# Kernel tuning notes

Measured on AMD Instinct MI355X. Metric: run time of the kernel, lower is better.

Reference implementation:

```python
import jax, jax.numpy as jnp
import numpy as np

H, L, N = 512, 4096, 64

def make_dplr_hippo(n):
    # HiPPO-LegS -> NPLR -> DPLR diagonalization (numpy, init-time only)
    p0 = np.sqrt(1 + 2 * np.arange(n))
    A = p0[:, None] * p0[None, :]
    A = -(np.tril(A) - np.diag(np.arange(n)))
    p = np.sqrt(np.arange(n) + 0.5)
    b = np.sqrt(2 * np.arange(n) + 1.0)
    S = A + p[:, None] * p[None, :]
    Lambda_re = np.full(n, np.diagonal(S).mean())
    Lambda_im, V = np.linalg.eigh(S * -1j)
    Pc = V.conj().T @ p
    Bc = V.conj().T @ b
    return Lambda_re, Lambda_im, Pc, Bc

def setup_inputs() -> dict:
    key = jax.random.key(0)
    k_u, k_c, k_s = jax.random.split(key, 3)
    lr, li, Pc, Bc = make_dplr_hippo(N)
    tile = lambda v: jnp.tile(jnp.asarray(v, jnp.float32)[None, :], (H, 1))
    dt_min, dt_max = 0.001, 0.1
    log_step = (jax.random.uniform(k_s, (H, 1), jnp.float32)
                * (np.log(dt_max) - np.log(dt_min)) + np.log(dt_min))
    return {
        "u": jax.random.normal(k_u, (H, L), jnp.float32),
        "Lambda_re": tile(lr), "Lambda_im": tile(li),
        "P_re": tile(Pc.real), "P_im": tile(Pc.imag),
        "B_re": tile(Bc.real), "B_im": tile(Bc.imag),
        "C": jax.random.normal(k_c, (H, N, 2), jnp.float32) * (0.5 ** 0.5),
        "D": jnp.ones((H, 1), jnp.float32),
        "log_step": log_step,
    }

def reference(u, Lambda_re, Lambda_im, P_re, P_im, B_re, B_im, C, D, log_step):
    # u: [H, L]; all params leading dim H (vmapped channels)
    Lam = jnp.minimum(Lambda_re, -1e-4) + 1j * Lambda_im      # [H, N]
    P = P_re + 1j * P_im                                       # [H, N]
    B = B_re + 1j * B_im                                       # [H, N]
    Cc = C[..., 0] + 1j * C[..., 1]                             # [H, N]
    step = jnp.exp(log_step)                                    # [H, 1]
    Lseq = u.shape[-1]
    Omega = jnp.exp(-2j * jnp.pi * (jnp.arange(Lseq) / Lseq)).astype(jnp.complex64)  # [L]
    g = (2.0 / step) * ((1.0 - Omega) / (1.0 + Omega))[None, :]  # [H, L]
    c = 2.0 / (1.0 + Omega)                                      # [L]
    denom = 1.0 / (g[:, :, None] - Lam[:, None, :])              # [H, L, N]
    cauchy = lambda v: jnp.einsum('hn,hln->hl', v, denom)
    k00 = cauchy(Cc.conj() * B)
    k01 = cauchy(Cc.conj() * P)
    k10 = cauchy(P.conj() * B)
    k11 = cauchy(P.conj() * P)
    atRoots = c[None, :] * (k00 - k01 * (1.0 / (1.0 + k11)) * k10)
    K = jnp.fft.ifft(atRoots, Lseq, axis=-1).real                # [H, L] conv kernel
    # causal convolution via zero-padded FFT (length 2L)
    ud = jnp.fft.rfft(u, n=2 * Lseq, axis=-1)
    Kd = jnp.fft.rfft(K, n=2 * Lseq, axis=-1)
    y = jnp.fft.irfft(ud * Kd, n=2 * Lseq, axis=-1)[..., :Lseq]
    return y + D * u
```

## Files before the change

kernel.cpp:

```cpp
#include <hip/hip_runtime.h>
#include <math.h>

#define NT 512

typedef float v2 __attribute__((ext_vector_type(2)));

__device__ __forceinline__ v2 vrot(v2 a){ return (v2){-a.y, a.x}; }
__device__ __forceinline__ v2 vconj(v2 a){ return (v2){a.x, -a.y}; }
__device__ __forceinline__ v2 vcmul(v2 a, v2 b){ return a.x*b + a.y*vrot(b); }
__device__ __forceinline__ v2 vfma1(float s, v2 v, v2 acc){
    return (v2){ __builtin_fmaf(s, v.x, acc.x), __builtin_fmaf(s, v.y, acc.y) };
}

__device__ __forceinline__ int SW(int e){ return e ^ (((e>>5) ^ (e>>9)) & 15); }

__device__ __forceinline__ int d8r4(int x){
    return ((x&7)<<9) | (((x>>3)&7)<<6) | (((x>>6)&7)<<3) | ((x>>9)&7);
}

__device__ __forceinline__ void dft8_inv(v2 t[8], v2 y[8]) {
    const float RH = 0.70710678f;
    v2 p  = t[0]+t[4], m  = t[0]-t[4], q  = t[2]+t[6], r  = t[2]-t[6];
    v2 rr = vrot(r);
    v2 E0 = p+q, E2 = p-q, E1 = m+rr, E3 = m-rr;
    v2 p2 = t[1]+t[5], m2 = t[1]-t[5], q2 = t[3]+t[7], r2 = t[3]-t[7];
    v2 rr2 = vrot(r2);
    v2 O0 = p2+q2, O2 = p2-q2, O1 = m2+rr2, O3 = m2-rr2;
    v2 W1O = RH*(O1 + vrot(O1));
    v2 W2O = vrot(O2);
    v2 W3O = vrot(RH*(O3 + vrot(O3)));
    y[0] = E0 + O0;  y[4] = E0 - O0;
    y[1] = E1 + W1O; y[5] = E1 - W1O;
    y[2] = E2 + W2O; y[6] = E2 - W2O;
    y[3] = E3 + W3O; y[7] = E3 - W3O;
}

__device__ __forceinline__ void dft8_fwd(v2 t[8], v2 y[8]) {
    const float RH = 0.70710678f;
    v2 p  = t[0]+t[4], m  = t[0]-t[4], q  = t[2]+t[6], r  = t[2]-t[6];
    v2 rr = vrot(r);
    v2 E0 = p+q, E2 = p-q, E1 = m-rr, E3 = m+rr;
    v2 p2 = t[1]+t[5], m2 = t[1]-t[5], q2 = t[3]+t[7], r2 = t[3]-t[7];
    v2 rr2 = vrot(r2);
    v2 O0 = p2+q2, O2 = p2-q2, O1 = m2-rr2, O3 = m2+rr2;
    v2 W1O = RH*(O1 - vrot(O1));
    v2 W2O = (v2){O2.y, -O2.x};
    v2 W3O = (-RH)*(O3 + vrot(O3));
    y[0] = E0 + O0;  y[4] = E0 - O0;
    y[1] = E1 + W1O; y[5] = E1 - W1O;
    y[2] = E2 + W2O; y[6] = E2 - W2O;
    y[3] = E3 + W3O; y[7] = E3 - W3O;
}

template<int Q, bool TW>
__device__ __forceinline__ void r8_dit_inv(v2* buf, int tid) {
    int j = tid & (Q-1);
    int base = 8*tid - 7*j;
    v2 t[8];
    #pragma unroll
    for (int k = 0; k < 8; ++k) t[k] = buf[SW(base + k*Q)];
    if (TW) {
        const float fm = 6.2831853072f / (float)(8*Q);
        float sb, cb; __sincosf(fm*(float)j, &sb, &cb);
        v2 W1 = (v2){cb, sb};
        v2 W2 = vcmul(W1,W1), W3 = vcmul(W1,W2), W4 = vcmul(W2,W2),
           W5 = vcmul(W2,W3), W6 = vcmul(W3,W3), W7 = vcmul(W3,W4);
        t[1]=vcmul(t[1],W1); t[2]=vcmul(t[2],W2); t[3]=vcmul(t[3],W3);
        t[4]=vcmul(t[4],W4); t[5]=vcmul(t[5],W5); t[6]=vcmul(t[6],W6);
        t[7]=vcmul(t[7],W7);
    }
    v2 y[8];
    dft8_inv(t, y);
    #pragma unroll
    for (int m = 0; m < 8; ++m) buf[SW(base + m*Q)] = y[m];
    __syncthreads();
}

template<int Q>
__device__ __forceinline__ void r8_dif_fwd(v2* buf, int tid) {
    int j = tid & (Q-1);
    int baseL = 8*tid - 7*j;
    v2 W1=(v2){1.0f,0.0f},W2=W1,W3=W1,W4=W1,W5=W1,W6=W1,W7=W1;
    if (Q > 1) {
        const float fm = -6.2831853072f / (float)(8*Q);
        float sb, cb; __sincosf(fm*(float)j, &sb, &cb);
        W1 = (v2){cb, sb};
        W2 = vcmul(W1,W1); W3 = vcmul(W1,W2); W4 = vcmul(W2,W2);
        W5 = vcmul(W2,W3); W6 = vcmul(W3,W3); W7 = vcmul(W3,W4);
    }
    #pragma unroll 1
    for (int hh = 0; hh < 2; ++hh) {
        int base = baseL + (hh << 12);
        v2 t[8];
        #pragma unroll
        for (int k = 0; k < 8; ++k) t[k] = buf[SW(base + k*Q)];
        v2 y[8];
        dft8_fwd(t, y);
        if (Q > 1) {
            y[1]=vcmul(y[1],W1); y[2]=vcmul(y[2],W2); y[3]=vcmul(y[3],W3);
            y[4]=vcmul(y[4],W4); y[5]=vcmul(y[5],W5); y[6]=vcmul(y[6],W6);
            y[7]=vcmul(y[7],W7);
        }
        #pragma unroll
        for (int m = 0; m < 8; ++m) buf[SW(base + m*Q)] = y[m];
    }
    __syncthreads();
}

__global__ void __launch_bounds__(NT)
s4_fused(const float* __restrict__ u,
         const float* __restrict__ Lre, const float* __restrict__ Lim,
         const float* __restrict__ Pre, const float* __restrict__ Pim,
         const float* __restrict__ Bre, const float* __restrict__ Bim,
         const float* __restrict__ Cin, const float* __restrict__ Din,
         const float* __restrict__ logstep,
         float* __restrict__ out)
{
    __shared__ v2 buf[8192];
    const int tid = threadIdx.x;
    const int h = blockIdx.x;

    v2* par = buf + 4096;
    if (tid < 64) {
        const int n = tid;
        float lre = fminf(Lre[h*64+n], -1e-4f);
        float lim = Lim[h*64+n];
        par[n] = (v2){lre, lim};
        float pr = Pre[h*64+n], pi = Pim[h*64+n];
        float br = Bre[h*64+n], bi = Bim[h*64+n];
        float cr = Cin[h*128+2*n], ci = Cin[h*128+2*n+1];
        v2 cc = (v2){cr, -ci};
        par[64+n]  = vcmul(cc, (v2){br, bi});
        par[128+n] = vcmul(cc, (v2){pr, pi});
        v2 pc = (v2){pr, -pi};
        par[192+n] = vcmul(pc, (v2){br, bi});
        par[256+n] = (v2){pr*pr + pi*pi, 0.0f};
    }
    __syncthreads();

    const float step = expf(logstep[h]);
    const float tos  = 2.0f / step;

    #pragma unroll 1
    for (int hp = 0; hp < 2; ++hp) {
        v2 g[4], cf[4], k00[4], k01[4], k10[4], k11[4];
        const int lbase = hp*(4*NT);
        #pragma unroll
        for (int i = 0; i < 4; ++i) {
            int l = lbase + i*NT + tid;
            float ang = -6.2831855f * ((float)l * (1.0f/4096.0f));
            double ds, dc;
            sincos((double)ang, &ds, &dc);
            float Omx = (float)dc, Omy = (float)ds;
            float nx = 1.0f-Omx, ny = -Omy;
            float dx = 1.0f+Omx, dy =  Omy;
            float dinv = 1.0f/(dx*dx + dy*dy);
            g[i]  = (v2){tos*((nx*dx+ny*dy)*dinv), tos*((ny*dx-nx*dy)*dinv)};
            cf[i] = (v2){2.0f*dx*dinv, -2.0f*dy*dinv};
            k00[i]=(v2)(0.0f); k01[i]=(v2)(0.0f); k10[i]=(v2)(0.0f); k11[i]=(v2)(0.0f);
        }
        #pragma unroll 1
        for (int n = 0; n < 64; ++n) {
            v2 lam = par[n];
            v2 w00 = par[64+n], w01 = par[128+n], w10 = par[192+n];
            float w11r = par[256+n].x;
            #pragma unroll
            for (int i = 0; i < 4; ++i) {
                v2 d = g[i] - lam;
                float inv = __builtin_amdgcn_rcpf(d.x*d.x + d.y*d.y);
                v2 p  = d * inv;
                v2 cp = (v2){p.x, -p.y};
                v2 rp = (v2){p.y,  p.x};
                k00[i] = vfma1(w00.y, rp, vfma1(w00.x, cp, k00[i]));
                k01[i] = vfma1(w01.y, rp, vfma1(w01.x, cp, k01[i]));
                k10[i] = vfma1(w10.y, rp, vfma1(w10.x, cp, k10[i]));
                k11[i] = vfma1(w11r,  cp, k11[i]);
            }
        }
        #pragma unroll
        for (int i = 0; i < 4; ++i) {
            int l = lbase + i*NT + tid;
            v2 opk = (v2){1.0f + k11[i].x, k11[i].y};
            float iv = 1.0f/(opk.x*opk.x + opk.y*opk.y);
            v2 r11 = vconj(opk) * iv;
            v2 t  = vcmul(vcmul(k01[i], r11), k10[i]);
            buf[SW(d8r4(l))] = vcmul(cf[i], k00[i] - t);
        }
    }
    __syncthreads();

    r8_dit_inv<1,  false>(buf, tid);
    r8_dit_inv<8,  true >(buf, tid);
    r8_dit_inv<64, true >(buf, tid);
    r8_dit_inv<512,true >(buf, tid);

    {
        float kv[8], uval[8];
        #pragma unroll
        for (int i = 0; i < 8; ++i) {
            int l = i*NT + tid;
            kv[i]   = buf[SW(l)].x * (1.0f/4096.0f);
            uval[i] = u[h*4096 + l];
        }
        __syncthreads();
        #pragma unroll
        for (int i = 0; i < 8; ++i) {
            int l = i*NT + tid;
            buf[SW(l)]      = (v2){uval[i], kv[i]};
            buf[SW(l+4096)] = (v2)(0.0f);
        }
    }
    __syncthreads();

    {
        const float fm = -6.2831853072f / 8192.0f;
        #pragma unroll 1
        for (int i = 0; i < 8; ++i) {
            int j = i*NT + tid;
            float sb, cb; __sincosf(fm*(float)j, &sb, &cb);
            v2 W = (v2){cb, sb};
            int a0 = SW(j), a1 = SW(j+4096);
            v2 a = buf[a0], c = buf[a1];
            buf[a0] = a + c;
            buf[a1] = vcmul(a - c, W);
        }
        __syncthreads();
    }
    r8_dif_fwd<512>(buf, tid);
    r8_dif_fwd<64 >(buf, tid);
    r8_dif_fwd<8  >(buf, tid);
    r8_dif_fwd<1  >(buf, tid);

    {
        const float fm = 6.2831853072f / 8192.0f;
        v2 v[8];
        #pragma unroll 1
        for (int i = 0; i < 8; ++i) {
            int r  = i*NT + tid;
            float sw_, cw_; __sincosf(fm*(float)r, &sw_, &cw_);
            v2 cur = (v2){cw_, sw_};
            int k1 = r,        k1c = (8192 - r) & 8191;
            int k2 = r + 4096, k2c = 4096 - r;
            v2 za = buf[SW(((k1 &1)<<12) + d8r4(k1 >>1))];
            v2 zb = buf[SW(((k1c&1)<<12) + d8r4(k1c>>1))];
            v2 zc = buf[SW(((k2 &1)<<12) + d8r4(k2 >>1))];
            v2 zd = buf[SW(((k2c&1)<<12) + d8r4(k2c>>1))];
            v2 U1 = 0.5f*(za + vconj(zb));
            v2 K1 = -0.5f*vrot(za - vconj(zb));
            v2 Yr = vcmul(U1, K1);
            v2 U2 = 0.5f*(zc + vconj(zd));
            v2 K2 = -0.5f*vrot(zc - vconj(zd));
            v2 Ys = vcmul(U2, K2);
            v[i] = (Yr + Ys) + vrot(vcmul(cur, Yr - Ys));
        }
        __syncthreads();
        #pragma unroll
        for (int i = 0; i < 8; ++i) {
            int r = i*NT + tid;
            buf[SW(d8r4(r))] = v[i];
        }
        __syncthreads();
    }

    r8_dit_inv<1,  false>(buf, tid);
    r8_dit_inv<8,  true >(buf, tid);
    r8_dit_inv<64, true >(buf, tid);
    r8_dit_inv<512,true >(buf, tid);

    {
        const float Dh = Din[h];
        const float sc = 1.0f / 8192.0f;
        const v2* u2 = (const v2*)(u + h*4096);
        v2*     out2 = (v2*)(out + h*4096);
        #pragma unroll
        for (int i = 0; i < 4; ++i) {
            int n = i*NT + tid;
            v2 p  = buf[SW(n)];
            v2 uu = u2[n];
            out2[n] = sc*p + Dh*uu;
        }
    }
}

extern "C" void kernel_launch(void* const* d_in, const int* in_sizes, int n_in,
                              void* d_out, int out_size, void* d_ws, size_t ws_size,
                              hipStream_t stream)
{
    const float* u       = (const float*)d_in[0];
    const float* Lre     = (const float*)d_in[1];
    const float* Lim     = (const float*)d_in[2];
    const float* Pre     = (const float*)d_in[3];
    const float* Pim     = (const float*)d_in[4];
    const float* Bre     = (const float*)d_in[5];
    const float* Bim     = (const float*)d_in[6];
    const float* Cin     = (const float*)d_in[7];
    const float* Din     = (const float*)d_in[8];
    const float* logstep = (const float*)d_in[9];
    float* out = (float*)d_out;
    const int H = in_sizes[8];
    hipLaunchKernelGGL(s4_fused, dim3(H), dim3(NT), 0, stream,
                       u, Lre, Lim, Pre, Pim, Bre, Bim, Cin, Din, logstep, out);
}
```

Measured before the change: 173.3 us.

## Fuse first and last radix-8 FFT stages with adjacent register phases

The first inverse-FFT radix-8 stage now runs directly on register results from the Cauchy phase, so one shared-memory round trip and barrier go away. The last inverse stage is fused with the packing of u and the kernel into the 8192-point input, with the first DIF twiddle folded in. The final inverse FFT's last stage is fused with the output write. Per-iteration sincos calls are replaced by twiddle recurrences using a constant rotation, which saves transcendental work but may accumulate a little rounding error.

```diff
diff --git a/kernel.cpp b/kernel.cpp
--- a/kernel.cpp
+++ b/kernel.cpp
@@ -16,6 +16,9 @@
 
 __device__ __forceinline__ int d8r4(int x){
     return ((x&7)<<9) | (((x>>3)&7)<<6) | (((x>>6)&7)<<3) | ((x>>9)&7);
+}
+__device__ __forceinline__ int rev3(int t){
+    return ((t&7)<<6) | (t&56) | ((t>>6)&7);
 }
 
 __device__ __forceinline__ void dft8_inv(v2 t[8], v2 y[8]) {
@@ -52,23 +55,24 @@
     y[3] = E3 + W3O; y[7] = E3 - W3O;
 }
 
-template<int Q, bool TW>
+__device__ __forceinline__ void apply_tw_inv(v2 t[8], float fm, int j) {
+    float sb, cb; __sincosf(fm*(float)j, &sb, &cb);
+    v2 W1 = (v2){cb, sb};
+    v2 W2 = vcmul(W1,W1), W3 = vcmul(W1,W2), W4 = vcmul(W2,W2),
+       W5 = vcmul(W2,W3), W6 = vcmul(W3,W3), W7 = vcmul(W3,W4);
+    t[1]=vcmul(t[1],W1); t[2]=vcmul(t[2],W2); t[3]=vcmul(t[3],W3);
+    t[4]=vcmul(t[4],W4); t[5]=vcmul(t[5],W5); t[6]=vcmul(t[6],W6);
+    t[7]=vcmul(t[7],W7);
+}
+
+template<int Q>
 __device__ __forceinline__ void r8_dit_inv(v2* buf, int tid) {
     int j = tid & (Q-1);
     int base = 8*tid - 7*j;
     v2 t[8];
     #pragma unroll
     for (int k = 0; k < 8; ++k) t[k] = buf[SW(base + k*Q)];
-    if (TW) {
-        const float fm = 6.2831853072f / (float)(8*Q);
-        float sb, cb; __sincosf(fm*(float)j, &sb, &cb);
-        v2 W1 = (v2){cb, sb};
-        v2 W2 = vcmul(W1,W1), W3 = vcmul(W1,W2), W4 = vcmul(W2,W2),
-           W5 = vcmul(W2,W3), W6 = vcmul(W3,W3), W7 = vcmul(W3,W4);
-        t[1]=vcmul(t[1],W1); t[2]=vcmul(t[2],W2); t[3]=vcmul(t[3],W3);
-        t[4]=vcmul(t[4],W4); t[5]=vcmul(t[5],W5); t[6]=vcmul(t[6],W6);
-        t[7]=vcmul(t[7],W7);
-    }
+    apply_tw_inv(t, 6.2831853072f / (float)(8*Q), j);
     v2 y[8];
     dft8_inv(t, y);
     #pragma unroll
@@ -141,6 +145,7 @@
     const float step = expf(logstep[h]);
     const float tos  = 2.0f / step;
 
+    v2 a4[4];
     #pragma unroll 1
     for (int hp = 0; hp < 2; ++hp) {
         v2 g[4], cf[4], k00[4], k01[4], k10[4], k11[4];
@@ -179,66 +184,72 @@
         }
         #pragma unroll
         for (int i = 0; i < 4; ++i) {
-            int l = lbase + i*NT + tid;
             v2 opk = (v2){1.0f + k11[i].x, k11[i].y};
             float iv = 1.0f/(opk.x*opk.x + opk.y*opk.y);
             v2 r11 = vconj(opk) * iv;
             v2 t  = vcmul(vcmul(k01[i], r11), k10[i]);
-            buf[SW(d8r4(l))] = vcmul(cf[i], k00[i] - t);
-        }
-    }
-    __syncthreads();
-
-    r8_dit_inv<1,  false>(buf, tid);
-    r8_dit_inv<8,  true >(buf, tid);
-    r8_dit_inv<64, true >(buf, tid);
-    r8_dit_inv<512,true >(buf, tid);
-
+            v2 res = vcmul(cf[i], k00[i] - t);
+            if (hp == 0) buf[SW(tid + 512*i)] = res;
+            else         a4[i] = res;
+        }
+    }
     {
-        float kv[8], uval[8];
-        #pragma unroll
-        for (int i = 0; i < 8; ++i) {
-            int l = i*NT + tid;
-            kv[i]   = buf[SW(l)].x * (1.0f/4096.0f);
-            uval[i] = u[h*4096 + l];
-        }
+        v2 t[8];
+        #pragma unroll
+        for (int k = 0; k < 4; ++k) t[k] = buf[SW(tid + 512*k)];
+        #pragma unroll
+        for (int k = 0; k < 4; ++k) t[4+k] = a4[k];
         __syncthreads();
-        #pragma unroll
-        for (int i = 0; i < 8; ++i) {
-            int l = i*NT + tid;
-            buf[SW(l)]      = (v2){uval[i], kv[i]};
-            buf[SW(l+4096)] = (v2)(0.0f);
-        }
-    }
-    __syncthreads();
+        v2 y[8];
+        dft8_inv(t, y);
+        int tb8 = 8*rev3(tid);
+        #pragma unroll
+        for (int m = 0; m < 8; ++m) buf[SW(tb8 + m)] = y[m];
+    }
+    __syncthreads();
+
+    r8_dit_inv<8 >(buf, tid);
+    r8_dit_inv<64>(buf, tid);
 
     {
-        const float fm = -6.2831853072f / 8192.0f;
-        #pragma unroll 1
-        for (int i = 0; i < 8; ++i) {
-            int j = i*NT + tid;
-            float sb, cb; __sincosf(fm*(float)j, &sb, &cb);
-            v2 W = (v2){cb, sb};
-            int a0 = SW(j), a1 = SW(j+4096);
-            v2 a = buf[a0], c = buf[a1];
-            buf[a0] = a + c;
-            buf[a1] = vcmul(a - c, W);
-        }
+        v2 t[8];
+        #pragma unroll
+        for (int k = 0; k < 8; ++k) t[k] = buf[SW(tid + 512*k)];
+        apply_tw_inv(t, 6.2831853072f / 4096.0f, tid);
+        v2 y[8];
+        dft8_inv(t, y);
+        float uval[8];
+        const float* up = u + h*4096;
+        #pragma unroll
+        for (int m = 0; m < 8; ++m) uval[m] = up[tid + 512*m];
         __syncthreads();
-    }
+        float s2, c2; __sincosf(-6.2831853072f/8192.0f*(float)tid, &s2, &c2);
+        v2 cur = (v2){c2, s2};
+        const v2 C16n = (v2){0.92387953f, -0.38268343f};
+        #pragma unroll
+        for (int m = 0; m < 8; ++m) {
+            int l = tid + 512*m;
+            v2 z = (v2){uval[m], y[m].x * (1.0f/4096.0f)};
+            buf[SW(l)]      = z;
+            buf[SW(l+4096)] = vcmul(z, cur);
+            cur = vcmul(cur, C16n);
+        }
+    }
+    __syncthreads();
+
     r8_dif_fwd<512>(buf, tid);
     r8_dif_fwd<64 >(buf, tid);
     r8_dif_fwd<8  >(buf, tid);
     r8_dif_fwd<1  >(buf, tid);
 
     {
-        const float fm = 6.2831853072f / 8192.0f;
+        float sb, cb; __sincosf(6.2831853072f/8192.0f*(float)tid, &sb, &cb);
+        v2 cur = (v2){cb, sb};
+        const v2 C16p = (v2){0.92387953f, 0.38268343f};
         v2 v[8];
         #pragma unroll 1
         for (int i = 0; i < 8; ++i) {
             int r  = i*NT + tid;
-            float sw_, cw_; __sincosf(fm*(float)r, &sw_, &cw_);
-            v2 cur = (v2){cw_, sw_};
             int k1 = r,        k1c = (8192 - r) & 8191;
             int k2 = r + 4096, k2c = 4096 - r;
             v2 za = buf[SW(((k1 &1)<<12) + d8r4(k1 >>1))];
@@ -252,32 +263,35 @@
             v2 K2 = -0.5f*vrot(zc - vconj(zd));
             v2 Ys = vcmul(U2, K2);
             v[i] = (Yr + Ys) + vrot(vcmul(cur, Yr - Ys));
+            cur = vcmul(cur, C16p);
         }
         __syncthreads();
-        #pragma unroll
-        for (int i = 0; i < 8; ++i) {
-            int r = i*NT + tid;
-            buf[SW(d8r4(r))] = v[i];
-        }
-        __syncthreads();
-    }
-
-    r8_dit_inv<1,  false>(buf, tid);
-    r8_dit_inv<8,  true >(buf, tid);
-    r8_dit_inv<64, true >(buf, tid);
-    r8_dit_inv<512,true >(buf, tid);
+        v2 y[8];
+        dft8_inv(v, y);
+        int tb8 = 8*rev3(tid);
+        #pragma unroll
+        for (int m = 0; m < 8; ++m) buf[SW(tb8 + m)] = y[m];
+    }
+    __syncthreads();
+
+    r8_dit_inv<8 >(buf, tid);
+    r8_dit_inv<64>(buf, tid);
 
     {
+        v2 t[8];
+        #pragma unroll
+        for (int k = 0; k < 8; ++k) t[k] = buf[SW(tid + 512*k)];
+        apply_tw_inv(t, 6.2831853072f / 4096.0f, tid);
+        v2 y[8];
+        dft8_inv(t, y);
         const float Dh = Din[h];
         const float sc = 1.0f / 8192.0f;
         const v2* u2 = (const v2*)(u + h*4096);
         v2*     out2 = (v2*)(out + h*4096);
         #pragma unroll
-        for (int i = 0; i < 4; ++i) {
-            int n = i*NT + tid;
-            v2 p  = buf[SW(n)];
-            v2 uu = u2[n];
-            out2[n] = sc*p + Dh*uu;
+        for (int m = 0; m < 4; ++m) {
+            int n = tid + 512*m;
+            out2[n] = sc*y[m] + Dh*u2[n];
         }
     }
 }
```

New measurement: 171.9 us. Within noise of the previous version (-0.8%).
